# Kernel optimization log

Hardware: AMD Instinct MI355X
Metric: run time of the kernel (lower is better)

Reference implementation:

```python
import jax, jax.numpy as jnp
import numpy as np

B, T, C = 8, 2048, 1024
EXP = 4
EPS = 1e-6


def rmsnorm(x, w):
    xf = x.astype(jnp.float32)
    y = xf * jax.lax.rsqrt(jnp.mean(xf * xf, axis=-1, keepdims=True) + EPS)
    return y.astype(x.dtype) * w


def setup_inputs() -> dict:
    key = jax.random.key(0)
    ks = jax.random.split(key, 8)
    x = jax.random.normal(ks[0], (B, T, C), dtype=jnp.float32)
    norm1_w = jnp.ones((C,), jnp.float32)
    norm2_w = jnp.ones((C,), jnp.float32)
    s1 = 1.0 / np.sqrt(C)
    s2 = 1.0 / np.sqrt(EXP * C)
    mlp1_w = jax.random.uniform(ks[1], (C, C), jnp.float32, -s1, s1)  # stored (in,out)
    mlp1_b = jax.random.uniform(ks[2], (C,), jnp.float32, -s1, s1)
    mlp2_w1 = jax.random.uniform(ks[3], (C, EXP * C), jnp.float32, -s1, s1)
    mlp2_b1 = jax.random.uniform(ks[4], (EXP * C,), jnp.float32, -s1, s1)
    mlp2_w2 = jax.random.uniform(ks[5], (EXP * C, C), jnp.float32, -s2, s2)
    mlp2_b2 = jax.random.uniform(ks[6], (C,), jnp.float32, -s2, s2)
    return {"x": x, "norm1_w": norm1_w, "mlp1_w": mlp1_w, "mlp1_b": mlp1_b,
            "norm2_w": norm2_w, "mlp2_w1": mlp2_w1, "mlp2_b1": mlp2_b1,
            "mlp2_w2": mlp2_w2, "mlp2_b2": mlp2_b2}


def reference(x, norm1_w, mlp1_w, mlp1_b, norm2_w, mlp2_w1, mlp2_b1, mlp2_w2, mlp2_b2):
    Tdim = x.shape[-2]
    # linear-RNN cumulative state with triangular-number scaler (faithful to source)
    state = jnp.cumsum(rmsnorm(x, norm1_w), axis=1)
    scaler = jnp.cumsum(jnp.arange(1, Tdim + 1, dtype=x.dtype))[None, :, None]
    state = state / scaler
    gate = jax.nn.sigmoid(jnp.einsum('btc,cd->btd', state, mlp1_w) + mlp1_b)
    out = gate * x
    h = rmsnorm(out, norm2_w)
    h = jax.nn.relu(jnp.einsum('btc,ce->bte', h, mlp2_w1) + mlp2_b1)
    out = jnp.einsum('bte,ec->btc', h, mlp2_w2) + mlp2_b2 + out
    return out
```

## Files before the change

### kernel.cpp

```cpp
#include <hip/hip_runtime.h>

__device__ __forceinline__ float bf2f(unsigned short u) {
    union { unsigned int i; float f; } v;
    v.i = ((unsigned int)u) << 16;
    return v.f;
}
__device__ __forceinline__ unsigned short f2bf(float f) {
    union { float f; unsigned int i; } v;
    v.f = f;
    unsigned int r = (v.i + 0x7fffu + ((v.i >> 16) & 1u)) >> 16;
    return (unsigned short)r;
}

typedef __attribute__((ext_vector_type(8))) short short8;
typedef __attribute__((ext_vector_type(4))) float floatx4;

#define GLOBAL_AS __attribute__((address_space(1)))
#define LDS_AS __attribute__((address_space(3)))

static constexpr int Bdim = 8;
static constexpr int Tdim = 2048;
static constexpr int Cdim = 1024;
static constexpr int Edim = 4096;
static constexpr int Mdim = Bdim * Tdim;

__global__ __launch_bounds__(256) void transpose_f2b(
    const float* __restrict__ src, unsigned short* __restrict__ dst, int K, int N) {
    __shared__ float tile[32][33];
    int n0 = blockIdx.x * 32;
    int k0 = blockIdx.y * 32;
    int tx = threadIdx.x & 31;
    int ty = threadIdx.x >> 5;
#pragma unroll
    for (int i = 0; i < 32; i += 8)
        tile[ty + i][tx] = src[(size_t)(k0 + ty + i) * N + n0 + tx];
    __syncthreads();
#pragma unroll
    for (int i = 0; i < 32; i += 8)
        dst[(size_t)(n0 + ty + i) * K + k0 + tx] = f2bf(tile[tx][ty + i]);
}

__global__ __launch_bounds__(256) void rms_inv_kernel(
    const float* __restrict__ x, float* __restrict__ rinv) {
    int row = blockIdx.x;
    int tid = threadIdx.x;
    float4 v = ((const float4*)(x + (size_t)row * Cdim))[tid];
    float s = v.x * v.x + v.y * v.y + v.z * v.z + v.w * v.w;
#pragma unroll
    for (int o = 32; o > 0; o >>= 1) s += __shfl_down(s, o, 64);
    __shared__ float ps[4];
    if ((tid & 63) == 0) ps[tid >> 6] = s;
    __syncthreads();
    if (tid == 0) {
        float tot = ps[0] + ps[1] + ps[2] + ps[3];
        rinv[row] = rsqrtf(tot * (1.0f / (float)Cdim) + 1e-6f);
    }
}

__global__ __launch_bounds__(256) void chunk_sums(
    const float* __restrict__ x, const float* __restrict__ rinv,
    const float* __restrict__ w, float* __restrict__ P) {
    int idx = blockIdx.x;
    int cb = idx & 3;
    int k = (idx >> 2) & 31;
    int b = idx >> 7;
    int c = cb * 256 + threadIdx.x;
    float wc = w[c];
    const float* base = x + ((size_t)b * Tdim + k * 64) * Cdim + c;
    const float* rbase = rinv + (size_t)b * Tdim + k * 64;
    float s = 0.f;
#pragma unroll 8
    for (int t = 0; t < 64; t++) s += base[(size_t)t * Cdim] * rbase[t];
    P[((size_t)b * 32 + k) * Cdim + c] = s * wc;
}

__global__ __launch_bounds__(256) void chunk_scan(float* __restrict__ P) {
    int g = blockIdx.x * 256 + threadIdx.x;
    int b = g >> 10;
    int c = g & 1023;
    float* p = P + (size_t)b * 32 * Cdim + c;
    float run = 0.f;
#pragma unroll
    for (int k = 0; k < 32; k++) {
        float v = p[(size_t)k * Cdim];
        p[(size_t)k * Cdim] = run;
        run += v;
    }
}

__global__ __launch_bounds__(256) void cumsum_state(
    const float* __restrict__ x, const float* __restrict__ rinv,
    const float* __restrict__ w, const float* __restrict__ P,
    unsigned short* __restrict__ state) {
    int idx = blockIdx.x;
    int cb = idx & 3;
    int k = (idx >> 2) & 31;
    int b = idx >> 7;
    int c = cb * 256 + threadIdx.x;
    float wc = w[c];
    float acc = P[((size_t)b * 32 + k) * Cdim + c];
    const float* base = x + ((size_t)b * Tdim + k * 64) * Cdim + c;
    const float* rbase = rinv + (size_t)b * Tdim + k * 64;
    unsigned short* sbase = state + ((size_t)b * Tdim + k * 64) * Cdim + c;
#pragma unroll 4
    for (int t = 0; t < 64; t++) {
        acc += base[(size_t)t * Cdim] * rbase[t] * wc;
        int tt = k * 64 + t;
        float inv = 2.0f / ((float)(tt + 1) * (float)(tt + 2));
        sbase[(size_t)t * Cdim] = f2bf(acc * inv);
    }
}

__global__ __launch_bounds__(256) void rmsnorm_f2b(
    const float* __restrict__ x, const float* __restrict__ w,
    unsigned short* __restrict__ y) {
    int row = blockIdx.x;
    int tid = threadIdx.x;
    float4 v = ((const float4*)(x + (size_t)row * Cdim))[tid];
    float s = v.x * v.x + v.y * v.y + v.z * v.z + v.w * v.w;
#pragma unroll
    for (int o = 32; o > 0; o >>= 1) s += __shfl_down(s, o, 64);
    __shared__ float ps[4];
    if ((tid & 63) == 0) ps[tid >> 6] = s;
    __syncthreads();
    float tot = ps[0] + ps[1] + ps[2] + ps[3];
    float r = rsqrtf(tot * (1.0f / (float)Cdim) + 1e-6f);
    float4 w4 = ((const float4*)w)[tid];
    ushort4 o;
    o.x = f2bf(v.x * r * w4.x);
    o.y = f2bf(v.y * r * w4.y);
    o.z = f2bf(v.z * r * w4.z);
    o.w = f2bf(v.w * r * w4.w);
    ((ushort4*)(y + (size_t)row * Cdim))[tid] = o;
}

template <int EPI>
__global__ __launch_bounds__(512, 2) void gemm8(
    const unsigned short* __restrict__ A, const unsigned short* __restrict__ BT,
    const float* __restrict__ bias, const float* __restrict__ extra,
    void* __restrict__ Coutv, int N, int K) {
    __shared__ __attribute__((aligned(16))) unsigned short As[2][256 * 64];
    __shared__ __attribute__((aligned(16))) unsigned short Bs[2][256 * 64];

    int tid = threadIdx.x;
    int nbn = N >> 8;
    int id = blockIdx.x;
    int nwg = gridDim.x;
    if ((nwg & 7) == 0) id = (id & 7) * (nwg >> 3) + (id >> 3);
    int bn = id % nbn;
    int bm = id / nbn;

    int lane = tid & 63;
    int w = tid >> 6;
    int wm = w >> 2;
    int wn = w & 3;
    int lrow = lane & 15;
    int l4 = lane >> 4;
    int swz = lrow & 7;
    int wmB = wm * 128, wnB = wn * 64;

    const unsigned short* Abase = A + (size_t)bm * 256 * K;
    const unsigned short* Bbase = BT + (size_t)bn * 256 * K;

    int sr = tid >> 3;
    int col8 = (tid & 7) ^ (sr & 7);

#define STAGE_A(sb, u, k0)                                                               \
    __builtin_amdgcn_global_load_lds(                                                    \
        (const GLOBAL_AS void*)(Abase + (size_t)((u) * 64 + sr) * K + (k0) + col8 * 8),  \
        (LDS_AS void*)(As[sb] + (u) * 4096 + tid * 8), 16, 0, 0)
#define STAGE_B(sb, u, k0)                                                               \
    __builtin_amdgcn_global_load_lds(                                                    \
        (const GLOBAL_AS void*)(Bbase + (size_t)((u) * 64 + sr) * K + (k0) + col8 * 8),  \
        (LDS_AS void*)(Bs[sb] + (u) * 4096 + tid * 8), 16, 0, 0)

#define LDA(cb, i, ks)                                                                   \
    (*(const short8*)(As[cb] + (wmB + (i) * 16 + lrow) * 64 + ((((ks) * 4 + l4) ^ swz) << 3)))
#define LDB(cb, jj, ks)                                                                  \
    (*(const short8*)(Bs[cb] + (wnB + (jj) * 16 + lrow) * 64 + ((((ks) * 4 + l4) ^ swz) << 3)))

#define PH_IN                                                                            \
    do {                                                                                 \
        __builtin_amdgcn_s_barrier();                                                    \
        asm volatile("s_waitcnt lgkmcnt(0)" ::: "memory");                               \
        __builtin_amdgcn_s_setprio(1);                                                   \
    } while (0)
#define PH_OUT                                                                           \
    do {                                                                                 \
        __builtin_amdgcn_s_setprio(0);                                                   \
        __builtin_amdgcn_s_barrier();                                                    \
    } while (0)

    floatx4 acc[8][4] = {};
    int nt = K >> 6;
    int nIter = nt >> 1;

    STAGE_A(0, 0, 0); STAGE_A(0, 1, 0); STAGE_A(0, 2, 0); STAGE_A(0, 3, 0);
    STAGE_B(0, 0, 0); STAGE_B(0, 1, 0); STAGE_B(0, 2, 0); STAGE_B(0, 3, 0);
    STAGE_B(1, 0, 64); STAGE_B(1, 1, 64); STAGE_B(1, 2, 64); STAGE_B(1, 3, 64);
    asm volatile("s_waitcnt vmcnt(4)" ::: "memory");
    __builtin_amdgcn_s_barrier();

    for (int j = 0; j < nIter; ++j) {
        int k1 = (2 * j + 1) << 6;
        int k2 = (2 * j + 2) << 6;
        int k3 = (2 * j + 3) << 6;
        bool nl = (j + 1 < nIter);

        short8 av[4], b0[4], b1[4];

#pragma unroll
        for (int i = 0; i < 4; i++) av[i] = LDA(0, i, 0);
#pragma unroll
        for (int i = 0; i < 4; i++) b0[i] = LDB(0, i, 0);
        STAGE_A(1, 0, k1); STAGE_A(1, 1, k1);
        PH_IN;
#pragma unroll
        for (int i = 0; i < 4; i++)
#pragma unroll
            for (int q = 0; q < 4; q++)
                acc[i][q] = __builtin_amdgcn_mfma_f32_16x16x32_bf16(av[i], b0[q], acc[i][q], 0, 0, 0);
        PH_OUT;

#pragma unroll
        for (int i = 0; i < 4; i++) av[i] = LDA(0, i, 1);
#pragma unroll
        for (int i = 0; i < 4; i++) b1[i] = LDB(0, i, 1);
        STAGE_A(1, 2, k1); STAGE_A(1, 3, k1);
        PH_IN;
#pragma unroll
        for (int i = 0; i < 4; i++)
#pragma unroll
            for (int q = 0; q < 4; q++)
                acc[i][q] = __builtin_amdgcn_mfma_f32_16x16x32_bf16(av[i], b1[q], acc[i][q], 0, 0, 0);
        PH_OUT;

#pragma unroll
        for (int i = 0; i < 4; i++) av[i] = LDA(0, 4 + i, 0);
        if (nl) { STAGE_B(0, 0, k2); STAGE_B(0, 1, k2); }
        PH_IN;
#pragma unroll
        for (int i = 0; i < 4; i++)
#pragma unroll
            for (int q = 0; q < 4; q++)
                acc[4 + i][q] = __builtin_amdgcn_mfma_f32_16x16x32_bf16(av[i], b0[q], acc[4 + i][q], 0, 0, 0);
        PH_OUT;

#pragma unroll
        for (int i = 0; i < 4; i++) av[i] = LDA(0, 4 + i, 1);
        if (nl) { STAGE_B(0, 2, k2); STAGE_B(0, 3, k2); }
        PH_IN;
#pragma unroll
        for (int i = 0; i < 4; i++)
#pragma unroll
            for (int q = 0; q < 4; q++)
                acc[4 + i][q] = __builtin_amdgcn_mfma_f32_16x16x32_bf16(av[i], b1[q], acc[4 + i][q], 0, 0, 0);
        __builtin_amdgcn_s_setprio(0);
        if (nl) asm volatile("s_waitcnt vmcnt(4)" ::: "memory");
        else    asm volatile("s_waitcnt vmcnt(0)" ::: "memory");
        __builtin_amdgcn_s_barrier();

#pragma unroll
        for (int i = 0; i < 4; i++) av[i] = LDA(1, i, 0);
#pragma unroll
        for (int i = 0; i < 4; i++) b0[i] = LDB(1, i, 0);
        if (nl) { STAGE_A(0, 0, k2); STAGE_A(0, 1, k2); }
        PH_IN;
#pragma unroll
        for (int i = 0; i < 4; i++)
#pragma unroll
            for (int q = 0; q < 4; q++)
                acc[i][q] = __builtin_amdgcn_mfma_f32_16x16x32_bf16(av[i], b0[q], acc[i][q], 0, 0, 0);
        PH_OUT;

#pragma unroll
        for (int i = 0; i < 4; i++) av[i] = LDA(1, i, 1);
#pragma unroll
        for (int i = 0; i < 4; i++) b1[i] = LDB(1, i, 1);
        if (nl) { STAGE_A(0, 2, k2); STAGE_A(0, 3, k2); }
        PH_IN;
#pragma unroll
        for (int i = 0; i < 4; i++)
#pragma unroll
            for (int q = 0; q < 4; q++)
                acc[i][q] = __builtin_amdgcn_mfma_f32_16x16x32_bf16(av[i], b1[q], acc[i][q], 0, 0, 0);
        PH_OUT;

#pragma unroll
        for (int i = 0; i < 4; i++) av[i] = LDA(1, 4 + i, 0);
        if (nl) { STAGE_B(1, 0, k3); STAGE_B(1, 1, k3); }
        PH_IN;
#pragma unroll
        for (int i = 0; i < 4; i++)
#pragma unroll
            for (int q = 0; q < 4; q++)
                acc[4 + i][q] = __builtin_amdgcn_mfma_f32_16x16x32_bf16(av[i], b0[q], acc[4 + i][q], 0, 0, 0);
        PH_OUT;

#pragma unroll
        for (int i = 0; i < 4; i++) av[i] = LDA(1, 4 + i, 1);
        if (nl) { STAGE_B(1, 2, k3); STAGE_B(1, 3, k3); }
        PH_IN;
#pragma unroll
        for (int i = 0; i < 4; i++)
#pragma unroll
            for (int q = 0; q < 4; q++)
                acc[4 + i][q] = __builtin_amdgcn_mfma_f32_16x16x32_bf16(av[i], b1[q], acc[4 + i][q], 0, 0, 0);
        __builtin_amdgcn_s_setprio(0);
        if (nl) asm volatile("s_waitcnt vmcnt(4)" ::: "memory");
        __builtin_amdgcn_s_barrier();
    }
#undef STAGE_A
#undef STAGE_B
#undef LDA
#undef LDB
#undef PH_IN
#undef PH_OUT

    int crow = l4 << 2;
    int ccol = lane & 15;
#pragma unroll
    for (int i = 0; i < 8; i++) {
#pragma unroll
        for (int q = 0; q < 4; q++) {
            size_t gm = (size_t)bm * 256 + wmB + i * 16 + crow;
            size_t gn = (size_t)bn * 256 + wnB + q * 16 + ccol;
            float bsv = bias[gn];
#pragma unroll
            for (int r = 0; r < 4; r++) {
                float v = acc[i][q][r] + bsv;
                size_t off = (gm + r) * (size_t)N + gn;
                if (EPI == 0) {
                    float g = 1.f / (1.f + __expf(-v));
                    ((float*)Coutv)[off] = g * extra[off];
                } else if (EPI == 1) {
                    ((unsigned short*)Coutv)[off] = f2bf(v > 0.f ? v : 0.f);
                } else {
                    ((float*)Coutv)[off] = v + extra[off];
                }
            }
        }
    }
}

extern "C" void kernel_launch(void* const* d_in, const int* in_sizes, int n_in,
                              void* d_out, int out_size, void* d_ws, size_t ws_size,
                              hipStream_t stream) {
    const float* x   = (const float*)d_in[0];
    const float* n1w = (const float*)d_in[1];
    const float* w1  = (const float*)d_in[2];
    const float* b1  = (const float*)d_in[3];
    const float* n2w = (const float*)d_in[4];
    const float* w21 = (const float*)d_in[5];
    const float* b21 = (const float*)d_in[6];
    const float* w22 = (const float*)d_in[7];
    const float* b22 = (const float*)d_in[8];
    float* out = (float*)d_out;

    char* ws = (char*)d_ws;
    const size_t MB = 1024ull * 1024ull;
    unsigned short* state = (unsigned short*)(ws);
    unsigned short* w1T   = (unsigned short*)(ws + 32 * MB);
    unsigned short* w21T  = (unsigned short*)(ws + 34 * MB);
    unsigned short* w22T  = (unsigned short*)(ws + 42 * MB);
    float* P              = (float*)(ws + 50 * MB);
    float* rinv           = (float*)(ws + 51 * MB);
    unsigned short* h     = (unsigned short*)(ws + 52 * MB);
    float* out1 = out;

    int slice_rows = Mdim;
    while (52 * MB + (size_t)slice_rows * Edim * 2 > ws_size && slice_rows > 1024)
        slice_rows >>= 1;

    transpose_f2b<<<dim3(Cdim / 32, Cdim / 32), 256, 0, stream>>>(w1, w1T, Cdim, Cdim);
    transpose_f2b<<<dim3(Edim / 32, Cdim / 32), 256, 0, stream>>>(w21, w21T, Cdim, Edim);
    transpose_f2b<<<dim3(Cdim / 32, Edim / 32), 256, 0, stream>>>(w22, w22T, Edim, Cdim);

    rms_inv_kernel<<<Mdim, 256, 0, stream>>>(x, rinv);

    chunk_sums<<<1024, 256, 0, stream>>>(x, rinv, n1w, P);
    chunk_scan<<<32, 256, 0, stream>>>(P);
    cumsum_state<<<1024, 256, 0, stream>>>(x, rinv, n1w, P, state);

    gemm8<0><<<dim3((Mdim / 256) * (Cdim / 256)), 512, 0, stream>>>(
        state, w1T, b1, x, out1, Cdim, Cdim);

    rmsnorm_f2b<<<Mdim, 256, 0, stream>>>(out1, n2w, state);

    for (int m0 = 0; m0 < Mdim; m0 += slice_rows) {
        gemm8<1><<<dim3((slice_rows / 256) * (Edim / 256)), 512, 0, stream>>>(
            state + (size_t)m0 * Cdim, w21T, b21, nullptr, h, Edim, Cdim);
        gemm8<2><<<dim3((slice_rows / 256) * (Cdim / 256)), 512, 0, stream>>>(
            h, w22T, b22, out1 + (size_t)m0 * Cdim, out + (size_t)m0 * Cdim,
            Cdim, Edim);
    }
}
```

Baseline: 561.8 us.

## Software-pipeline LDS fragment loads ahead of MFMA phases, halve barriers

Restructures the GEMM main loop so LDS fragment reads for the next MFMA phase are issued before the current phase's MFMAs. It uses separate register sets a0..a3 in place of one reused av buffer and partial lgkmcnt waits. Each phase now has one barrier instead of two, and the global-to-LDS staging order and vmcnt thresholds are reshuffled to match. The aim is to hide LDS latency behind matrix-core work and cut synchronisation overhead. The cost is higher VGPR pressure and tighter correctness reasoning around buffer reuse and the reordered wait counts.

```diff
diff --git a/kernel.cpp b/kernel.cpp
--- a/kernel.cpp
+++ b/kernel.cpp
@@ -179,16 +179,16 @@
 #define LDB(cb, jj, ks)                                                                  \
     (*(const short8*)(Bs[cb] + (wnB + (jj) * 16 + lrow) * 64 + ((((ks) * 4 + l4) ^ swz) << 3)))
 
-#define PH_IN                                                                            \
+#define BAR __builtin_amdgcn_s_barrier()
+#define LGK(n) asm volatile("s_waitcnt lgkmcnt(" #n ")" ::: "memory")
+#define MM(R, AV, BV)                                                                    \
     do {                                                                                 \
-        __builtin_amdgcn_s_barrier();                                                    \
-        asm volatile("s_waitcnt lgkmcnt(0)" ::: "memory");                               \
         __builtin_amdgcn_s_setprio(1);                                                   \
-    } while (0)
-#define PH_OUT                                                                           \
-    do {                                                                                 \
+        _Pragma("unroll") for (int i_ = 0; i_ < 4; i_++)                                 \
+            _Pragma("unroll") for (int q_ = 0; q_ < 4; q_++)                             \
+                acc[(R) + i_][q_] = __builtin_amdgcn_mfma_f32_16x16x32_bf16(             \
+                    AV[i_], BV[q_], acc[(R) + i_][q_], 0, 0, 0);                         \
         __builtin_amdgcn_s_setprio(0);                                                   \
-        __builtin_amdgcn_s_barrier();                                                    \
     } while (0)
 
     floatx4 acc[8][4] = {};
@@ -199,7 +199,7 @@
     STAGE_B(0, 0, 0); STAGE_B(0, 1, 0); STAGE_B(0, 2, 0); STAGE_B(0, 3, 0);
     STAGE_B(1, 0, 64); STAGE_B(1, 1, 64); STAGE_B(1, 2, 64); STAGE_B(1, 3, 64);
     asm volatile("s_waitcnt vmcnt(4)" ::: "memory");
-    __builtin_amdgcn_s_barrier();
+    BAR;
 
     for (int j = 0; j < nIter; ++j) {
         int k1 = (2 * j + 1) << 6;
@@ -207,115 +207,77 @@
         int k3 = (2 * j + 3) << 6;
         bool nl = (j + 1 < nIter);
 
-        short8 av[4], b0[4], b1[4];
-
-#pragma unroll
-        for (int i = 0; i < 4; i++) av[i] = LDA(0, i, 0);
-#pragma unroll
-        for (int i = 0; i < 4; i++) b0[i] = LDB(0, i, 0);
+        short8 a0[4], a1[4], a2[4], a3[4], b0[4], b1[4];
+
+#pragma unroll
+        for (int i = 0; i < 4; i++) a0[i] = LDA(0, i, 0);
+#pragma unroll
+        for (int q = 0; q < 4; q++) b0[q] = LDB(0, q, 0);
+#pragma unroll
+        for (int i = 0; i < 4; i++) a1[i] = LDA(0, 4 + i, 0);
         STAGE_A(1, 0, k1); STAGE_A(1, 1, k1);
-        PH_IN;
-#pragma unroll
-        for (int i = 0; i < 4; i++)
-#pragma unroll
-            for (int q = 0; q < 4; q++)
-                acc[i][q] = __builtin_amdgcn_mfma_f32_16x16x32_bf16(av[i], b0[q], acc[i][q], 0, 0, 0);
-        PH_OUT;
-
-#pragma unroll
-        for (int i = 0; i < 4; i++) av[i] = LDA(0, i, 1);
-#pragma unroll
-        for (int i = 0; i < 4; i++) b1[i] = LDB(0, i, 1);
+        BAR;
+        MM(0, a0, b0);
+
+#pragma unroll
+        for (int i = 0; i < 4; i++) a2[i] = LDA(0, i, 1);
+#pragma unroll
+        for (int q = 0; q < 4; q++) b1[q] = LDB(0, q, 1);
         STAGE_A(1, 2, k1); STAGE_A(1, 3, k1);
-        PH_IN;
-#pragma unroll
-        for (int i = 0; i < 4; i++)
-#pragma unroll
-            for (int q = 0; q < 4; q++)
-                acc[i][q] = __builtin_amdgcn_mfma_f32_16x16x32_bf16(av[i], b1[q], acc[i][q], 0, 0, 0);
-        PH_OUT;
-
-#pragma unroll
-        for (int i = 0; i < 4; i++) av[i] = LDA(0, 4 + i, 0);
+        BAR;
+        MM(4, a1, b0);
+
+#pragma unroll
+        for (int i = 0; i < 4; i++) a3[i] = LDA(0, 4 + i, 1);
+        LGK(4);
+        BAR;
+        MM(0, a2, b1);
+
         if (nl) { STAGE_B(0, 0, k2); STAGE_B(0, 1, k2); }
-        PH_IN;
-#pragma unroll
-        for (int i = 0; i < 4; i++)
-#pragma unroll
-            for (int q = 0; q < 4; q++)
-                acc[4 + i][q] = __builtin_amdgcn_mfma_f32_16x16x32_bf16(av[i], b0[q], acc[4 + i][q], 0, 0, 0);
-        PH_OUT;
-
-#pragma unroll
-        for (int i = 0; i < 4; i++) av[i] = LDA(0, 4 + i, 1);
-        if (nl) { STAGE_B(0, 2, k2); STAGE_B(0, 3, k2); }
-        PH_IN;
-#pragma unroll
-        for (int i = 0; i < 4; i++)
-#pragma unroll
-            for (int q = 0; q < 4; q++)
-                acc[4 + i][q] = __builtin_amdgcn_mfma_f32_16x16x32_bf16(av[i], b1[q], acc[4 + i][q], 0, 0, 0);
-        __builtin_amdgcn_s_setprio(0);
+        LGK(0);
+        if (nl) asm volatile("s_waitcnt vmcnt(2)" ::: "memory");
+        else    asm volatile("s_waitcnt vmcnt(0)" ::: "memory");
+        BAR;
+        MM(4, a3, b1);
+
+#pragma unroll
+        for (int i = 0; i < 4; i++) a0[i] = LDA(1, i, 0);
+#pragma unroll
+        for (int q = 0; q < 4; q++) b0[q] = LDB(1, q, 0);
+#pragma unroll
+        for (int i = 0; i < 4; i++) a1[i] = LDA(1, 4 + i, 0);
+        if (nl) { STAGE_B(0, 2, k2); STAGE_B(0, 3, k2); STAGE_A(0, 0, k2); STAGE_A(0, 1, k2); }
+        BAR;
+        MM(0, a0, b0);
+
+#pragma unroll
+        for (int i = 0; i < 4; i++) a2[i] = LDA(1, i, 1);
+#pragma unroll
+        for (int q = 0; q < 4; q++) b1[q] = LDB(1, q, 1);
+        if (nl) { STAGE_A(0, 2, k2); STAGE_A(0, 3, k2); }
+        BAR;
+        MM(4, a1, b0);
+
+#pragma unroll
+        for (int i = 0; i < 4; i++) a3[i] = LDA(1, 4 + i, 1);
+        LGK(4);
+        BAR;
+        MM(0, a2, b1);
+
+        if (nl) { STAGE_B(1, 0, k3); STAGE_B(1, 1, k3); STAGE_B(1, 2, k3); STAGE_B(1, 3, k3); }
+        LGK(0);
         if (nl) asm volatile("s_waitcnt vmcnt(4)" ::: "memory");
         else    asm volatile("s_waitcnt vmcnt(0)" ::: "memory");
-        __builtin_amdgcn_s_barrier();
-
-#pragma unroll
-        for (int i = 0; i < 4; i++) av[i] = LDA(1, i, 0);
-#pragma unroll
-        for (int i = 0; i < 4; i++) b0[i] = LDB(1, i, 0);
-        if (nl) { STAGE_A(0, 0, k2); STAGE_A(0, 1, k2); }
-        PH_IN;
-#pragma unroll
-        for (int i = 0; i < 4; i++)
-#pragma unroll
-            for (int q = 0; q < 4; q++)
-                acc[i][q] = __builtin_amdgcn_mfma_f32_16x16x32_bf16(av[i], b0[q], acc[i][q], 0, 0, 0);
-        PH_OUT;
-
-#pragma unroll
-        for (int i = 0; i < 4; i++) av[i] = LDA(1, i, 1);
-#pragma unroll
-        for (int i = 0; i < 4; i++) b1[i] = LDB(1, i, 1);
-        if (nl) { STAGE_A(0, 2, k2); STAGE_A(0, 3, k2); }
-        PH_IN;
-#pragma unroll
-        for (int i = 0; i < 4; i++)
-#pragma unroll
-            for (int q = 0; q < 4; q++)
-                acc[i][q] = __builtin_amdgcn_mfma_f32_16x16x32_bf16(av[i], b1[q], acc[i][q], 0, 0, 0);
-        PH_OUT;
-
-#pragma unroll
-        for (int i = 0; i < 4; i++) av[i] = LDA(1, 4 + i, 0);
-        if (nl) { STAGE_B(1, 0, k3); STAGE_B(1, 1, k3); }
-        PH_IN;
-#pragma unroll
-        for (int i = 0; i < 4; i++)
-#pragma unroll
-            for (int q = 0; q < 4; q++)
-                acc[4 + i][q] = __builtin_amdgcn_mfma_f32_16x16x32_bf16(av[i], b0[q], acc[4 + i][q], 0, 0, 0);
-        PH_OUT;
-
-#pragma unroll
-        for (int i = 0; i < 4; i++) av[i] = LDA(1, 4 + i, 1);
-        if (nl) { STAGE_B(1, 2, k3); STAGE_B(1, 3, k3); }
-        PH_IN;
-#pragma unroll
-        for (int i = 0; i < 4; i++)
-#pragma unroll
-            for (int q = 0; q < 4; q++)
-                acc[4 + i][q] = __builtin_amdgcn_mfma_f32_16x16x32_bf16(av[i], b1[q], acc[4 + i][q], 0, 0, 0);
-        __builtin_amdgcn_s_setprio(0);
-        if (nl) asm volatile("s_waitcnt vmcnt(4)" ::: "memory");
-        __builtin_amdgcn_s_barrier();
+        BAR;
+        MM(4, a3, b1);
     }
 #undef STAGE_A
 #undef STAGE_B
 #undef LDA
 #undef LDB
-#undef PH_IN
-#undef PH_OUT
+#undef BAR
+#undef LGK
+#undef MM
 
     int crow = l4 << 2;
     int ccol = lane & 15;
```

After: 776.7 us. 1.38x slower.
